# Kernel optimization log

Measured on AMD Instinct MI355X. Metric: run time of the kernel, lower is better.

The kernel has to match this reference:

```python
import jax, jax.numpy as jnp
import numpy as np

# dims
B, S, V, H, D, I, L, SL, P = 1, 2048, 32000, 1024, 512, 4096, 2, 32, 4096
DECAY_FAST, DECAY_SLOW, CONS_RATE, CONS_EVERY = 0.9, 0.99, 0.1, 10


def _ln(x, g, b):
    m = x.mean(-1, keepdims=True)
    v = ((x - m) ** 2).mean(-1, keepdims=True)
    return (x - m) * jax.lax.rsqrt(v + 1e-5) * g + b


def _memory_scan(items, gates, fast0, slow0):
    # items [B,S,D], gates [B,S,SL]; sequential per-timestep memory update
    cons = (jnp.arange(items.shape[1]) % CONS_EVERY) == 0
    def step(carry, x):
        fast, slow = carry
        item, gate, c = x
        fast = DECAY_FAST * fast + gate[:, :, None] * item[:, None, :]
        slow = jnp.where(c, DECAY_SLOW * slow + CONS_RATE * fast, slow)
        fast = jnp.where(c, (1.0 - CONS_RATE) * fast, fast)
        return (fast, slow), None
    (fast, slow), _ = jax.lax.scan(
        step, (fast0, slow0),
        (items.transpose(1, 0, 2), gates.transpose(1, 0, 2), cons))
    return fast, slow


def _forward(input_ids, fast_states, slow_states, emb, pos_emb, W_item, b_item,
             W_q, b_q, rh_W1, rh_b1, rh_W2, rh_b2, gate_W, gate_b, W_out, b_out,
             ln1_g, ln1_b, ffn_W1, ffn_b1, ffn_W2, ffn_b2, ln2_g, ln2_b, fln_g, fln_b):
    b, s = input_ids.shape
    h = emb[input_ids] + pos_emb[:s][None]  # [B,S,H]
    new_fast, new_slow = [], []
    for l in range(W_item.shape[0]):
        items = h @ W_item[l] + b_item[l]          # [B,S,D]
        query = h @ W_q[l] + b_q[l]                # [B,S,H]
        # retrieval head -> unit-norm unbinding keys
        k1 = jax.nn.gelu(items @ rh_W1[l] + rh_b1[l])
        keys = k1 @ rh_W2[l] + rh_b2[l]
        keys = keys / (jnp.linalg.norm(keys, axis=-1, keepdims=True) + 1e-6)
        fast0, slow0 = fast_states[l], slow_states[l]  # [B,SL,D]
        # retrieval uses the initial (constant-within-sequence) states, so it
        # vectorizes over seq: slot attention + hadamard unbinding
        mem = jnp.concatenate([fast0, slow0], axis=1)  # [B,2*SL,D]
        scores = jnp.einsum('bsd,bnd->bsn', keys, mem) / jnp.sqrt(jnp.float32(D))
        attn = jax.nn.softmax(scores, axis=-1)
        retrieved = jnp.einsum('bsn,bnd->bsd', attn, mem) * keys  # [B,S,D]
        gates = jax.nn.sigmoid(jnp.concatenate([h, retrieved], -1) @ gate_W[l] + gate_b[l])
        fast_gates = gates[..., :SL]
        fast, slow = _memory_scan(items, fast_gates, fast0, slow0)
        new_fast.append(fast)
        new_slow.append(slow)
        out = jnp.concatenate([query, retrieved], -1) @ W_out[l] + b_out[l]
        h = _ln(h + out, ln1_g[l], ln1_b[l])
        ffn = jax.nn.gelu(h @ ffn_W1[l] + ffn_b1[l]) @ ffn_W2[l] + ffn_b2[l]
        h = _ln(h + ffn, ln2_g[l], ln2_b[l])
    h = _ln(h, fln_g, fln_b)
    logits = jnp.einsum('bsh,vh->bsv', h, emb)  # tied lm_head
    return logits, jnp.stack(new_fast), jnp.stack(new_slow)


def setup_inputs() -> dict:
    key = jax.random.key(0)
    def rn(i, shape, scale=0.02):
        return jax.random.normal(jax.random.fold_in(key, i), shape, dtype=jnp.float32) * scale
    z = lambda shape: jnp.zeros(shape, jnp.float32)
    return dict(
        input_ids=jax.random.randint(jax.random.fold_in(key, 0), (B, S), 0, V),
        fast_states=rn(100, (L, B, SL, D), 0.5),
        slow_states=rn(101, (L, B, SL, D), 0.5),
        emb=rn(1, (V, H)),
        pos_emb=rn(2, (P, H)),
        W_item=rn(3, (L, H, D)), b_item=z((L, D)),
        W_q=rn(4, (L, H, H)), b_q=z((L, H)),
        rh_W1=rn(5, (L, D, 2 * D)), rh_b1=z((L, 2 * D)),
        rh_W2=rn(6, (L, 2 * D, D)), rh_b2=z((L, D)),
        gate_W=rn(7, (L, H + D, 2 * SL)), gate_b=z((L, 2 * SL)),
        W_out=rn(8, (L, H + D, H)), b_out=z((L, H)),
        ln1_g=jnp.ones((L, H)), ln1_b=z((L, H)),
        ffn_W1=rn(9, (L, H, I)), ffn_b1=z((L, I)),
        ffn_W2=rn(10, (L, I, H)), ffn_b2=z((L, H)),
        ln2_g=jnp.ones((L, H)), ln2_b=z((L, H)),
        fln_g=jnp.ones((H,)), fln_b=z((H,)),
    )


def reference(input_ids, fast_states, slow_states, emb, pos_emb, W_item, b_item,
              W_q, b_q, rh_W1, rh_b1, rh_W2, rh_b2, gate_W, gate_b, W_out, b_out,
              ln1_g, ln1_b, ffn_W1, ffn_b1, ffn_W2, ffn_b2, ln2_g, ln2_b, fln_g, fln_b):
    return _forward(input_ids, fast_states, slow_states, emb, pos_emb, W_item, b_item,
                    W_q, b_q, rh_W1, rh_b1, rh_W2, rh_b2, gate_W, gate_b, W_out, b_out,
                    ln1_g, ln1_b, ffn_W1, ffn_b1, ffn_W2, ffn_b2, ln2_g, ln2_b, fln_g, fln_b)
```

## Files before the change

### kernel.cpp

```cpp
#include <hip/hip_runtime.h>
#include <hip/hip_bf16.h>
#include <stdint.h>

typedef __hip_bfloat16 bf16;
typedef float f32x4 __attribute__((ext_vector_type(4)));
typedef short s16x8 __attribute__((ext_vector_type(8)));
typedef short s16x4 __attribute__((ext_vector_type(4)));

#define DEV __device__ __forceinline__

static constexpr int S_ = 2048, H_ = 1024, D_ = 512, I_ = 4096, V_ = 32000;
static constexpr int SLn = 32, Lc = 2;
static constexpr size_t LOGITS_N = (size_t)S_ * V_;

DEV float gelu_f(float x) {
    float x3 = x * x * x;
    return 0.5f * x * (1.f + tanhf(0.7978845608028654f * (x + 0.044715f * x3)));
}

#define AS1(p) ((const __attribute__((address_space(1))) void*)(uintptr_t)(p))
#define AS3(p) ((__attribute__((address_space(3))) void*)(uint32_t)(uintptr_t)(p))

__global__ __launch_bounds__(512, 1) void logits_gemm(const bf16* __restrict__ A,
                                                      const bf16* __restrict__ BT,
                                                      float* __restrict__ C) {
    constexpr int NT = 32;
    __shared__ short lds[4 * 16384];
    const int tid = threadIdx.x, lane = tid & 63;
    const int wid = tid >> 6;
    const int wm = wid >> 2, wn = wid & 3;

    int bid = blockIdx.x;
    int wgid = (bid & 7) * 125 + (bid >> 3);
    const int m0 = (wgid & 7) * 256;
    const int n0 = (wgid >> 3) * 256;

    const int L = tid * 16;
    const int sidx = L >> 10, w = L & 1023;
    const int r16 = w >> 6;
    const int c2 = (w & 63) ^ (((r16 >> 3) & 1) << 5);
    const int srow = sidx * 16 + r16;
    const int scol = c2 >> 1;
    const bf16* aSrc[2];
    const bf16* bSrc[2];
#pragma unroll
    for (int h = 0; h < 2; ++h) {
        aSrc[h] = A + (size_t)(m0 + h * 128 + srow) * 1536 + scol;
        bSrc[h] = BT + (size_t)(n0 + h * 128 + srow) * 1024 + scol;
    }
    auto STA = [&](int kt, int h) {
        __builtin_amdgcn_global_load_lds(AS1(aSrc[h] + kt * 32),
                                         AS3(&lds[(kt & 3) * 16384 + h * 4096 + tid * 8]), 16, 0, 0);
    };
    auto STB = [&](int kt, int h) {
        __builtin_amdgcn_global_load_lds(AS1(bSrc[h] + kt * 32),
                                         AS3(&lds[(kt & 3) * 16384 + 8192 + h * 4096 + tid * 8]), 16, 0, 0);
    };

    const int laneoff = (lane & 15) * 32 + (((lane >> 4) * 8) ^ (((lane >> 3) & 1) << 4));

    f32x4 acc[8][4];
#pragma unroll
    for (int i = 0; i < 8; i++)
#pragma unroll
        for (int j = 0; j < 4; j++)
#pragma unroll
            for (int r = 0; r < 4; r++) acc[i][j][r] = 0.f;

    s16x8 a0[4], a1[4], b0[4], b1[4];
    auto rdA = [&](s16x8(&d)[4], int kt, int mq) {
        const short* p = &lds[(kt & 3) * 16384 + wm * 4096 + mq * 2048];
#pragma unroll
        for (int f = 0; f < 4; ++f) d[f] = *(const s16x8*)&p[f * 512 + laneoff];
    };
    auto rdB = [&](s16x8(&d)[4], int kt) {
        const short* p = &lds[(kt & 3) * 16384 + 8192 + wn * 2048];
#pragma unroll
        for (int j = 0; j < 4; ++j) d[j] = *(const s16x8*)&p[j * 512 + laneoff];
    };
    auto MM = [&](int mq, s16x8(&a)[4], s16x8(&b)[4]) {
        __builtin_amdgcn_s_setprio(1);
#pragma unroll
        for (int f = 0; f < 4; ++f)
#pragma unroll
            for (int j = 0; j < 4; ++j)
                acc[mq * 4 + f][j] =
                    __builtin_amdgcn_mfma_f32_16x16x32_bf16(a[f], b[j], acc[mq * 4 + f][j], 0, 0, 0);
        __builtin_amdgcn_s_setprio(0);
    };

#define GATE(tight)                                                     \
    do {                                                                \
        __builtin_amdgcn_s_barrier();                                   \
        if (tight) asm volatile("s_waitcnt vmcnt(0)" ::: "memory");     \
        else       asm volatile("s_waitcnt vmcnt(4)" ::: "memory");     \
        asm volatile("s_waitcnt lgkmcnt(0)" ::: "memory");              \
        __builtin_amdgcn_sched_barrier(0);                              \
    } while (0)
#define SB() __builtin_amdgcn_sched_barrier(0)

#pragma unroll
    for (int kt = 0; kt < 3; ++kt) {
        STA(kt, 0); STA(kt, 1); STB(kt, 0); STB(kt, 1);
    }
    asm volatile("s_waitcnt vmcnt(4)" ::: "memory");
    __builtin_amdgcn_s_barrier();
    rdA(a0, 0, 0);
    rdB(b0, 0);

    for (int tt = 0; tt < NT; tt += 2) {
        {
            const int t = tt;
            const bool tight = (t >= NT - 2);
            GATE(tight);
            rdA(a1, t, 1);
            SB();
            MM(0, a0, b0);
            if (t + 3 < NT) { STA(t + 3, 0); STA(t + 3, 1); }
            GATE(tight);
            if (t + 1 < NT) { rdA(a0, t + 1, 0); rdB(b1, t + 1); }
            SB();
            MM(1, a1, b0);
            if (t + 3 < NT) { STB(t + 3, 0); STB(t + 3, 1); }
        }
        {
            const int t = tt + 1;
            const bool tight = (t >= NT - 2);
            GATE(tight);
            rdA(a1, t, 1);
            SB();
            MM(0, a0, b1);
            if (t + 3 < NT) { STA(t + 3, 0); STA(t + 3, 1); }
            GATE(tight);
            if (t + 1 < NT) { rdA(a0, t + 1, 0); rdB(b0, t + 1); }
            SB();
            MM(1, a1, b1);
            if (t + 3 < NT) { STB(t + 3, 0); STB(t + 3, 1); }
        }
    }
#undef GATE
#undef SB

#pragma unroll
    for (int i = 0; i < 8; i++) {
        int gr0 = m0 + wm * 128 + i * 16 + ((lane >> 4) << 2);
#pragma unroll
        for (int j = 0; j < 4; j++) {
            int gc = n0 + wn * 64 + j * 16 + (lane & 15);
#pragma unroll
            for (int r = 0; r < 4; r++) C[(size_t)(gr0 + r) * V_ + gc] = acc[i][j][r];
        }
    }
}

template <int BM, int BN, int TH, int WM, int WN, int FLAGS>
__global__ __launch_bounds__(TH, 3) void gemm_p5(
    const bf16* __restrict__ A, int lda, const bf16* __restrict__ BT,
    const float* __restrict__ bias, const float* __restrict__ bias2,
    float* __restrict__ Cf, int ldf, bf16* __restrict__ Cb, int ldb2,
    bf16* __restrict__ Cb2, int K, int Mt, int Nt) {
    constexpr int FM = BM / (WM * 16), FN = BN / (WN * 16);
    constexpr int CA = (BM * 4) / TH, CB = (BN * 4) / TH, CH = CA + CB;
    constexpr int NPH = (FM * FN >= 32) ? 2 : 1;
    constexpr int FMP = FM / NPH;
    constexpr int BUFS = (BM + BN) * 32;
    __shared__ short lds[4 * BUFS];
    const int tid = threadIdx.x, lane = tid & 63;
    const int wm = (tid >> 6) / WN, wn = (tid >> 6) % WN;

    int nwg = Mt * Nt;
    int bid = blockIdx.x, wgid = bid;
    if ((nwg & 7) == 0) {
        int cpx = nwg >> 3;
        wgid = (bid & 7) * cpx + (bid >> 3);
    }
    const int m0 = (wgid % Mt) * BM, n0 = (wgid / Mt) * BN;

    const bf16* aS[CA];
    const bf16* bS[CB];
#pragma unroll
    for (int c = 0; c < CA; ++c) {
        int L = (c * TH + tid) * 16;
        int sidx = L >> 10, w = L & 1023;
        int r16 = w >> 6;
        int c2 = (w & 63) ^ (((r16 >> 3) & 1) << 5);
        aS[c] = A + (size_t)(m0 + sidx * 16 + r16) * lda + (c2 >> 1);
    }
#pragma unroll
    for (int c = 0; c < CB; ++c) {
        int L = (c * TH + tid) * 16;
        int sidx = L >> 10, w = L & 1023;
        int r16 = w >> 6;
        int c2 = (w & 63) ^ (((r16 >> 3) & 1) << 5);
        bS[c] = BT + (size_t)(n0 + sidx * 16 + r16) * K + (c2 >> 1);
    }

    auto stageA = [&](int kt) {
        short* dst = &lds[(kt & 3) * BUFS];
#pragma unroll
        for (int c = 0; c < CA; ++c)
            __builtin_amdgcn_global_load_lds(AS1(aS[c] + kt * 32), AS3(dst + (c * TH + tid) * 8), 16, 0, 0);
    };
    auto stageB = [&](int kt) {
        short* dst = &lds[(kt & 3) * BUFS + BM * 32];
#pragma unroll
        for (int c = 0; c < CB; ++c)
            __builtin_amdgcn_global_load_lds(AS1(bS[c] + kt * 32), AS3(dst + (c * TH + tid) * 8), 16, 0, 0);
    };

    const int laneoff = ((lane & 15) * 64 + ((((lane >> 4) * 8) ^ (((lane >> 3) & 1) << 4)) << 1)) >> 1;

    f32x4 acc[FM][FN];
#pragma unroll
    for (int i = 0; i < FM; i++)
#pragma unroll
        for (int j = 0; j < FN; j++)
#pragma unroll
            for (int r = 0; r < 4; r++) acc[i][j][r] = 0.f;

    const int NT = K >> 5;
    stageA(0); stageB(0);
    stageA(1); stageB(1);
    stageA(2); stageB(2);
    asm volatile("s_waitcnt vmcnt(%0)" ::"n"(2 * CH) : "memory");
    __builtin_amdgcn_s_barrier();
    for (int t = 0; t < NT; ++t) {
        const short* as = &lds[(t & 3) * BUFS];
        const short* bs = as + BM * 32;
        s16x8 bf[FN];
#pragma unroll
        for (int p = 0; p < NPH; ++p) {
            s16x8 af[FMP];
#pragma unroll
            for (int i = 0; i < FMP; i++)
                af[i] = *(const s16x8*)&as[(wm * FM + p * FMP + i) * 512 + laneoff];
            if (p == 0) {
#pragma unroll
                for (int j = 0; j < FN; j++)
                    bf[j] = *(const s16x8*)&bs[(wn * FN + j) * 512 + laneoff];
            }
            if (t + 3 < NT) {
                if (NPH == 1) {
                    stageA(t + 3);
                    stageB(t + 3);
                } else if (p == 0) {
                    stageA(t + 3);
                } else {
                    stageB(t + 3);
                }
            }
            if (p == NPH - 1) {
                const int rem = NT - 1 - t;
                if (rem >= 3)
                    asm volatile("s_waitcnt vmcnt(%0)" ::"n"(2 * CH) : "memory");
                else if (rem == 2)
                    asm volatile("s_waitcnt vmcnt(%0)" ::"n"(CH) : "memory");
                else
                    asm volatile("s_waitcnt vmcnt(0)" ::: "memory");
            }
            __builtin_amdgcn_s_barrier();
            __builtin_amdgcn_sched_barrier(0);
            __builtin_amdgcn_s_setprio(1);
#pragma unroll
            for (int i = 0; i < FMP; i++)
#pragma unroll
                for (int j = 0; j < FN; j++)
                    acc[p * FMP + i][j] =
                        __builtin_amdgcn_mfma_f32_16x16x32_bf16(af[i], bf[j], acc[p * FMP + i][j], 0, 0, 0);
            __builtin_amdgcn_s_setprio(0);
            __builtin_amdgcn_s_barrier();
        }
    }

#pragma unroll
    for (int i = 0; i < FM; i++) {
        int gr0 = m0 + (wm * FM + i) * 16 + ((lane >> 4) << 2);
#pragma unroll
        for (int j = 0; j < FN; j++) {
            int gc = n0 + (wn * FN + j) * 16 + (lane & 15);
            if (FLAGS & 32) {
                if (gc < 512) {
                    float bv = bias[gc];
#pragma unroll
                    for (int r = 0; r < 4; r++) {
                        float v = acc[i][j][r] + bv;
                        Cf[(size_t)(gr0 + r) * 512 + gc] = v;
                        Cb2[(size_t)(gr0 + r) * 512 + gc] = __float2bfloat16(v);
                    }
                } else {
                    float bv = bias2[gc - 512];
#pragma unroll
                    for (int r = 0; r < 4; r++)
                        Cb[(size_t)(gr0 + r) * 1536 + (gc - 512)] = __float2bfloat16(acc[i][j][r] + bv);
                }
            } else {
                float bv = (FLAGS & 1) ? bias[gc] : 0.f;
#pragma unroll
                for (int r = 0; r < 4; r++) {
                    float v = acc[i][j][r] + bv;
                    if (FLAGS & 2) v = gelu_f(v);
                    if (FLAGS & 4) Cf[(size_t)(gr0 + r) * ldf + gc] = v;
                    if (FLAGS & 8) Cb[(size_t)(gr0 + r) * ldb2 + gc] = __float2bfloat16(v);
                }
            }
        }
    }
}

__global__ __launch_bounds__(256) void transpose_bf16_kernel(const float* __restrict__ W,
                                                             bf16* __restrict__ WT, int K, int N) {
    __shared__ float t[32][33];
    int tx = threadIdx.x & 31, ty = threadIdx.x >> 5;
    int kb = blockIdx.y * 32, nb = blockIdx.x * 32;
#pragma unroll
    for (int i = 0; i < 4; i++)
        t[ty + 8 * i][tx] = W[(size_t)(kb + ty + 8 * i) * N + nb + tx];
    __syncthreads();
#pragma unroll
    for (int i = 0; i < 4; i++)
        WT[(size_t)(nb + ty + 8 * i) * K + kb + tx] = __float2bfloat16(t[tx][ty + 8 * i]);
}

__global__ void conv_bf16_kernel(const float* __restrict__ src, bf16* __restrict__ dst) {
    size_t i = (size_t)blockIdx.x * 256 + threadIdx.x;
    f32x4 v = ((const f32x4*)src)[i];
    s16x4 o;
#pragma unroll
    for (int j = 0; j < 4; j++) {
        bf16 h = __float2bfloat16(v[j]);
        o[j] = *(short*)&h;
    }
    ((s16x4*)dst)[i] = o;
}

__global__ void embed_kernel(const int* __restrict__ ids, const float* __restrict__ emb,
                             const float* __restrict__ pos, float* __restrict__ hF,
                             bf16* __restrict__ hB) {
    int t = blockIdx.x, tid = threadIdx.x;
    int id = ids[t];
    f32x4 v = ((const f32x4*)(emb + (size_t)id * H_))[tid];
    f32x4 q = ((const f32x4*)(pos + (size_t)t * H_))[tid];
    v = v + q;
    ((f32x4*)(hF + (size_t)t * H_))[tid] = v;
    s16x4 o;
#pragma unroll
    for (int j = 0; j < 4; j++) {
        bf16 h = __float2bfloat16(v[j]);
        o[j] = *(short*)&h;
    }
    ((s16x4*)(hB + (size_t)t * 1536))[tid] = o;
}

__global__ __launch_bounds__(256) void ln_kernel(const float* __restrict__ x,
                                                 const float* __restrict__ res,
                                                 const float* __restrict__ g,
                                                 const float* __restrict__ b,
                                                 float* __restrict__ of, bf16* __restrict__ ob,
                                                 int ldo) {
    __shared__ float red[8];
    int row = blockIdx.x, tid = threadIdx.x, lane = tid & 63, wid = tid >> 6;
    const float* xr = x + (size_t)row * H_;
    float v[4];
#pragma unroll
    for (int j = 0; j < 4; j++) {
        int c = tid + 256 * j;
        v[j] = xr[c] + (res ? res[(size_t)row * H_ + c] : 0.f);
    }
    float s = v[0] + v[1] + v[2] + v[3];
#pragma unroll
    for (int o = 32; o; o >>= 1) s += __shfl_xor(s, o);
    if (!lane) red[wid] = s;
    __syncthreads();
    float mean = (red[0] + red[1] + red[2] + red[3]) * (1.f / H_);
    float q = 0.f;
#pragma unroll
    for (int j = 0; j < 4; j++) {
        float d = v[j] - mean;
        q += d * d;
    }
#pragma unroll
    for (int o = 32; o; o >>= 1) q += __shfl_xor(q, o);
    if (!lane) red[4 + wid] = q;
    __syncthreads();
    float var = (red[4] + red[5] + red[6] + red[7]) * (1.f / H_);
    float rstd = rsqrtf(var + 1e-5f);
#pragma unroll
    for (int j = 0; j < 4; j++) {
        int c = tid + 256 * j;
        float o2 = (v[j] - mean) * rstd * g[c] + b[c];
        if (of) of[(size_t)row * H_ + c] = o2;
        if (ob) ob[(size_t)row * ldo + c] = __float2bfloat16(o2);
    }
}

__global__ void memt_kernel(const float* __restrict__ fast0, const float* __restrict__ slow0,
                            float* __restrict__ memT) {
    int idx = blockIdx.x * 256 + threadIdx.x;
    int d = idx >> 6, n = idx & 63;
    const float* m = (n < 32) ? fast0 + (size_t)n * D_ : slow0 + (size_t)(n - 32) * D_;
    memT[idx] = m[d];
}

__global__ __launch_bounds__(256) void attn_kernel(const float* __restrict__ keys,
                                                   const float* __restrict__ memT,
                                                   const float* __restrict__ fast0,
                                                   const float* __restrict__ slow0,
                                                   bf16* __restrict__ qr, bf16* __restrict__ hr) {
    __shared__ float klds[4][512];
    int wid = threadIdx.x >> 6, lane = threadIdx.x & 63;
    int r = blockIdx.x * 4 + wid;
    float kv[8], ss = 0.f;
#pragma unroll
    for (int j = 0; j < 8; j++) {
        kv[j] = keys[(size_t)r * D_ + lane + 64 * j];
        ss += kv[j] * kv[j];
    }
#pragma unroll
    for (int o = 32; o; o >>= 1) ss += __shfl_xor(ss, o);
    float inv = 1.f / (sqrtf(ss) + 1e-6f);
#pragma unroll
    for (int j = 0; j < 8; j++) {
        kv[j] *= inv;
        klds[wid][lane + 64 * j] = kv[j];
    }
    __syncthreads();
    float s0 = 0.f, s1 = 0.f, s2 = 0.f, s3 = 0.f;
#pragma unroll 8
    for (int d = 0; d < 512; d += 4) {
        s0 = fmaf(klds[wid][d + 0], memT[(d + 0) * 64 + lane], s0);
        s1 = fmaf(klds[wid][d + 1], memT[(d + 1) * 64 + lane], s1);
        s2 = fmaf(klds[wid][d + 2], memT[(d + 2) * 64 + lane], s2);
        s3 = fmaf(klds[wid][d + 3], memT[(d + 3) * 64 + lane], s3);
    }
    float s = (s0 + s1 + s2 + s3) * 0.044194173824159216f;
    float m = s;
#pragma unroll
    for (int o = 32; o; o >>= 1) m = fmaxf(m, __shfl_xor(m, o));
    float p = expf(s - m);
    float sum = p;
#pragma unroll
    for (int o = 32; o; o >>= 1) sum += __shfl_xor(sum, o);
    float pn = p / sum;
    float rv[8];
#pragma unroll
    for (int j = 0; j < 8; j++) rv[j] = 0.f;
    for (int n2 = 0; n2 < 64; ++n2) {
        float a2 = __shfl(pn, n2);
        const float* m2 = (n2 < 32) ? (fast0 + (size_t)n2 * D_) : (slow0 + (size_t)(n2 - 32) * D_);
#pragma unroll
        for (int j = 0; j < 8; j++) rv[j] = fmaf(a2, m2[lane + 64 * j], rv[j]);
    }
#pragma unroll
    for (int j = 0; j < 8; j++) {
        bf16 o = __float2bfloat16(rv[j] * kv[j]);
        qr[(size_t)r * 1536 + 1024 + lane + 64 * j] = o;
        hr[(size_t)r * 1536 + 1024 + lane + 64 * j] = o;
    }
}

__global__ void coef_kernel(float* __restrict__ coef) {
    int t = blockIdx.x * 256 + threadIdx.x;
    int j0 = (t + 9) / 10;
    float a = powf(0.9f, (float)(2047 - t + 205 - j0));
    float b = 0.f;
    for (int j = j0; j < 205; ++j)
        b += powf(0.9f, (float)(10 * j - t + j - j0)) * powf(0.99f, (float)(204 - j));
    b *= 0.1f;
    coef[t] = a;
    coef[2048 + t] = b;
    if (t == 0) {
        coef[4096] = powf(0.99f, 205.f);
        float cfs = 0.f;
        for (int j = 0; j < 205; ++j)
            cfs += powf(0.9f, (float)(11 * j + 1)) * powf(0.99f, (float)(204 - j));
        coef[4097] = 0.1f * cfs;
    }
}

__global__ void sigcoef_kernel(const float* __restrict__ raw, const float* __restrict__ coef,
                               float* __restrict__ ga, float* __restrict__ gb) {
    int i = blockIdx.x * 256 + threadIdx.x;
    int r = i >> 5, n = i & 31;
    float g = 1.f / (1.f + expf(-raw[r * 64 + n]));
    ga[i] = g * coef[r];
    gb[i] = g * coef[2048 + r];
}

__global__ __launch_bounds__(256) void scan_part_kernel(const float* __restrict__ items,
                                                        const float* __restrict__ ga,
                                                        const float* __restrict__ gb,
                                                        float* __restrict__ pF,
                                                        float* __restrict__ pS) {
    int tid = threadIdx.x;
    int d = (blockIdx.x & 7) * 64 + (tid & 63);
    int mg = (blockIdx.x >> 3) & 1;
    int tc = blockIdx.x >> 4;
    int m0 = mg * 16 + (tid >> 6) * 4;
    float aF[4] = {0.f, 0.f, 0.f, 0.f}, aS[4] = {0.f, 0.f, 0.f, 0.f};
    for (int t = tc * 128; t < tc * 128 + 128; ++t) {
        float it = items[(size_t)t * D_ + d];
#pragma unroll
        for (int j = 0; j < 4; j++) {
            aF[j] = fmaf(ga[t * 32 + m0 + j], it, aF[j]);
            aS[j] = fmaf(gb[t * 32 + m0 + j], it, aS[j]);
        }
    }
#pragma unroll
    for (int j = 0; j < 4; j++) {
        pF[((size_t)tc * 32 + m0 + j) * D_ + d] = aF[j];
        pS[((size_t)tc * 32 + m0 + j) * D_ + d] = aS[j];
    }
}

__global__ __launch_bounds__(256) void scan_reduce_kernel(const float* __restrict__ pF,
                                                          const float* __restrict__ pS,
                                                          const float* __restrict__ coef,
                                                          const float* __restrict__ fast0,
                                                          const float* __restrict__ slow0,
                                                          float* __restrict__ fastO,
                                                          float* __restrict__ slowO) {
    int i = blockIdx.x * 256 + threadIdx.x;
    float f = 0.f, s = 0.f;
#pragma unroll
    for (int c = 0; c < 16; c++) {
        f += pF[(size_t)c * 32 * D_ + i];
        s += pS[(size_t)c * 32 * D_ + i];
    }
    fastO[i] = f;
    slowO[i] = s + coef[4096] * slow0[i] + coef[4097] * fast0[i];
}

static inline void gemmM(hipStream_t st, const bf16* A, int lda, const bf16* BT,
                         const float* bias, const float* bias2, float* Cf, int ldf, bf16* Cb,
                         int ldb2, bf16* Cb2, int M, int N, int K, int flags) {
    if (N >= 1536 && (N % 128) == 0) {
        int Mt = M / 128, Nt = N / 128;
        dim3 g(Mt * Nt), b(256);
        if (flags == 33)
            gemm_p5<128, 128, 256, 2, 2, 33><<<g, b, 0, st>>>(A, lda, BT, bias, bias2, Cf, ldf,
                                                              Cb, ldb2, Cb2, K, Mt, Nt);
        else if (flags == 11)
            gemm_p5<128, 128, 256, 2, 2, 11><<<g, b, 0, st>>>(A, lda, BT, bias, bias2, Cf, ldf,
                                                              Cb, ldb2, Cb2, K, Mt, Nt);
        else
            gemm_p5<128, 128, 256, 2, 2, 5><<<g, b, 0, st>>>(A, lda, BT, bias, bias2, Cf, ldf,
                                                             Cb, ldb2, Cb2, K, Mt, Nt);
        return;
    }
    int Mt = M / 128, Nt = N / 64;
    dim3 g(Mt * Nt), b(256);
    if (flags == 11)
        gemm_p5<128, 64, 256, 2, 2, 11><<<g, b, 0, st>>>(A, lda, BT, bias, bias2, Cf, ldf, Cb,
                                                         ldb2, Cb2, K, Mt, Nt);
    else
        gemm_p5<128, 64, 256, 2, 2, 5><<<g, b, 0, st>>>(A, lda, BT, bias, bias2, Cf, ldf, Cb,
                                                        ldb2, Cb2, K, Mt, Nt);
}

static inline void transp(hipStream_t st, const float* W, bf16* WT, int K, int N) {
    transpose_bf16_kernel<<<dim3(N / 32, K / 32), 256, 0, st>>>(W, WT, K, N);
}

extern "C" void kernel_launch(void* const* d_in, const int* in_sizes, int n_in,
                              void* d_out, int out_size, void* d_ws, size_t ws_size,
                              hipStream_t stream) {
    const int* ids = (const int*)d_in[0];
    const float* fastS = (const float*)d_in[1];
    const float* slowS = (const float*)d_in[2];
    const float* emb = (const float*)d_in[3];
    const float* pos = (const float*)d_in[4];
    const float* W_item = (const float*)d_in[5];
    const float* b_item = (const float*)d_in[6];
    const float* W_q = (const float*)d_in[7];
    const float* b_q = (const float*)d_in[8];
    const float* rh_W1 = (const float*)d_in[9];
    const float* rh_b1 = (const float*)d_in[10];
    const float* rh_W2 = (const float*)d_in[11];
    const float* rh_b2 = (const float*)d_in[12];
    const float* gate_W = (const float*)d_in[13];
    const float* gate_b = (const float*)d_in[14];
    const float* W_out = (const float*)d_in[15];
    const float* b_out = (const float*)d_in[16];
    const float* ln1_g = (const float*)d_in[17];
    const float* ln1_b = (const float*)d_in[18];
    const float* ffn_W1 = (const float*)d_in[19];
    const float* ffn_b1 = (const float*)d_in[20];
    const float* ffn_W2 = (const float*)d_in[21];
    const float* ffn_b2 = (const float*)d_in[22];
    const float* ln2_g = (const float*)d_in[23];
    const float* ln2_b = (const float*)d_in[24];
    const float* fln_g = (const float*)d_in[25];
    const float* fln_b = (const float*)d_in[26];
    float* outP = (float*)d_out;

    size_t off = 0;
    char* base = (char*)d_ws;
    auto alloc = [&](size_t n) -> char* {
        char* p = base + off;
        off += (n + 255) & ~(size_t)255;
        return p;
    };
    bf16* wIQ = (bf16*)alloc((size_t)Lc * 1536 * H_ * 2);
    bf16* rh1T = (bf16*)alloc((size_t)Lc * (2 * D_) * D_ * 2);
    bf16* rh2T = (bf16*)alloc((size_t)Lc * D_ * (2 * D_) * 2);
    bf16* wOutT = (bf16*)alloc((size_t)Lc * H_ * 1536 * 2);
    bf16* f1T = (bf16*)alloc((size_t)Lc * I_ * H_ * 2);
    bf16* f2T = (bf16*)alloc((size_t)Lc * H_ * I_ * 2);
    bf16* gWT = (bf16*)alloc((size_t)Lc * 64 * 1536 * 2);
    bf16* embB = (bf16*)alloc((size_t)V_ * H_ * 2);
    float* hF = (float*)alloc((size_t)S_ * H_ * 4);
    bf16* hrB = (bf16*)alloc((size_t)S_ * 1536 * 2);
    bf16* hB = hrB;
    float* itemsF = (float*)alloc((size_t)S_ * D_ * 4);
    bf16* itemsB = (bf16*)alloc((size_t)S_ * D_ * 2);
    bf16* qrB = (bf16*)alloc((size_t)S_ * 1536 * 2);
    bf16* k1B = (bf16*)alloc((size_t)S_ * (2 * D_) * 2);
    float* keysF = (float*)alloc((size_t)S_ * D_ * 4);
    float* outF = (float*)alloc((size_t)S_ * H_ * 4);
    bf16* ffn1B = (bf16*)alloc((size_t)S_ * I_ * 2);
    float* gRawF = (float*)alloc((size_t)S_ * 64 * 4);
    float* gaF = (float*)alloc((size_t)S_ * SLn * 4);
    float* gbF = (float*)alloc((size_t)S_ * SLn * 4);
    float* coefF = (float*)alloc(4200 * 4);
    float* memT = (float*)alloc((size_t)D_ * 64 * 4);
    float* pF = (float*)alloc((size_t)16 * SLn * D_ * 4);
    float* pS = (float*)alloc((size_t)16 * SLn * D_ * 4);

    coef_kernel<<<8, 256, 0, stream>>>(coefF);
    for (int l = 0; l < Lc; ++l) {
        transp(stream, W_item + (size_t)l * H_ * D_, wIQ + (size_t)l * 1536 * H_, H_, D_);
        transp(stream, W_q + (size_t)l * H_ * H_, wIQ + (size_t)l * 1536 * H_ + (size_t)512 * H_,
               H_, H_);
        transp(stream, rh_W1 + (size_t)l * D_ * 2 * D_, rh1T + (size_t)l * 2 * D_ * D_, D_, 2 * D_);
        transp(stream, rh_W2 + (size_t)l * 2 * D_ * D_, rh2T + (size_t)l * D_ * 2 * D_, 2 * D_, D_);
        transp(stream, W_out + (size_t)l * 1536 * H_, wOutT + (size_t)l * H_ * 1536, 1536, H_);
        transp(stream, ffn_W1 + (size_t)l * H_ * I_, f1T + (size_t)l * I_ * H_, H_, I_);
        transp(stream, ffn_W2 + (size_t)l * I_ * H_, f2T + (size_t)l * H_ * I_, I_, H_);
        transp(stream, gate_W + (size_t)l * 1536 * 64, gWT + (size_t)l * 64 * 1536, 1536, 64);
    }
    conv_bf16_kernel<<<(int)((size_t)V_ * H_ / 4 / 256), 256, 0, stream>>>(emb, embB);
    embed_kernel<<<S_, 256, 0, stream>>>(ids, emb, pos, hF, hB);

    for (int l = 0; l < Lc; ++l) {
        const float* fast0 = fastS + (size_t)l * SLn * D_;
        const float* slow0 = slowS + (size_t)l * SLn * D_;
        gemmM(stream, hB, 1536, wIQ + (size_t)l * 1536 * H_, b_item + l * D_, b_q + l * H_,
              itemsF, 512, qrB, 1536, itemsB, S_, 1536, H_, 33);
        gemmM(stream, itemsB, D_, rh1T + (size_t)l * 2 * D_ * D_, rh_b1 + l * 2 * D_, nullptr,
              nullptr, 0, k1B, 2 * D_, nullptr, S_, 2 * D_, D_, 11);
        gemmM(stream, k1B, 2 * D_, rh2T + (size_t)l * D_ * 2 * D_, rh_b2 + l * D_, nullptr,
              keysF, D_, nullptr, 0, nullptr, S_, D_, 2 * D_, 5);
        memt_kernel<<<128, 256, 0, stream>>>(fast0, slow0, memT);
        attn_kernel<<<S_ / 4, 256, 0, stream>>>(keysF, memT, fast0, slow0, qrB, hrB);
        gemmM(stream, hrB, 1536, gWT + (size_t)l * 64 * 1536, gate_b + l * 64, nullptr, gRawF,
              64, nullptr, 0, nullptr, S_, 64, 1536, 5);
        sigcoef_kernel<<<S_ * SLn / 256, 256, 0, stream>>>(gRawF, coefF, gaF, gbF);
        scan_part_kernel<<<256, 256, 0, stream>>>(itemsF, gaF, gbF, pF, pS);
        scan_reduce_kernel<<<64, 256, 0, stream>>>(
            pF, pS, coefF, fast0, slow0, outP + LOGITS_N + (size_t)l * SLn * D_,
            outP + LOGITS_N + (size_t)Lc * SLn * D_ + (size_t)l * SLn * D_);
        gemmM(stream, qrB, 1536, wOutT + (size_t)l * H_ * 1536, b_out + l * H_, nullptr, outF,
              H_, nullptr, 0, nullptr, S_, H_, 1536, 5);
        ln_kernel<<<S_, 256, 0, stream>>>(hF, outF, ln1_g + l * H_, ln1_b + l * H_, hF, hB, 1536);
        gemmM(stream, hB, 1536, f1T + (size_t)l * I_ * H_, ffn_b1 + l * I_, nullptr, nullptr, 0,
              ffn1B, I_, nullptr, S_, I_, H_, 11);
        gemmM(stream, ffn1B, I_, f2T + (size_t)l * H_ * I_, ffn_b2 + l * H_, nullptr, outF, H_,
              nullptr, 0, nullptr, S_, H_, I_, 5);
        ln_kernel<<<S_, 256, 0, stream>>>(hF, outF, ln2_g + l * H_, ln2_b + l * H_, hF, hB, 1536);
    }
    ln_kernel<<<S_, 256, 0, stream>>>(hF, nullptr, fln_g, fln_b, nullptr, hB, 1536);
    logits_gemm<<<1000, 512, 0, stream>>>(hB, embB, outP);
}
```

Measured before the change: 887.6 us.

## Restructure logits GEMM main loop to one barrier per k-tile with full-tile register double-buffering

The logits GEMM main loop now reads whole k-tiles (8 A fragments and 4 B fragments) into alternating even/odd register sets. Each k-tile gets one barrier/waitcnt gate instead of two half-tile gates. The A and B global-to-LDS loads for a stage are issued together. The vmcnt wait now comes before the barrier rather than after it. The aim is to cut synchronisation overhead and give longer uninterrupted MFMA runs, at the cost of more operand registers live at once and a coarser overlap between LDS reads and MFMAs.

```diff
diff --git a/kernel.cpp b/kernel.cpp
--- a/kernel.cpp
+++ b/kernel.cpp
@@ -48,13 +48,14 @@
         aSrc[h] = A + (size_t)(m0 + h * 128 + srow) * 1536 + scol;
         bSrc[h] = BT + (size_t)(n0 + h * 128 + srow) * 1024 + scol;
     }
-    auto STA = [&](int kt, int h) {
-        __builtin_amdgcn_global_load_lds(AS1(aSrc[h] + kt * 32),
-                                         AS3(&lds[(kt & 3) * 16384 + h * 4096 + tid * 8]), 16, 0, 0);
-    };
-    auto STB = [&](int kt, int h) {
-        __builtin_amdgcn_global_load_lds(AS1(bSrc[h] + kt * 32),
-                                         AS3(&lds[(kt & 3) * 16384 + 8192 + h * 4096 + tid * 8]), 16, 0, 0);
+    auto stage = [&](int kt) {
+#pragma unroll
+        for (int h = 0; h < 2; ++h) {
+            __builtin_amdgcn_global_load_lds(AS1(aSrc[h] + kt * 32),
+                                             AS3(&lds[(kt & 3) * 16384 + h * 4096 + tid * 8]), 16, 0, 0);
+            __builtin_amdgcn_global_load_lds(AS1(bSrc[h] + kt * 32),
+                                             AS3(&lds[(kt & 3) * 16384 + 8192 + h * 4096 + tid * 8]), 16, 0, 0);
+        }
     };
 
     const int laneoff = (lane & 15) * 32 + (((lane >> 4) * 8) ^ (((lane >> 3) & 1) << 4));
@@ -67,76 +68,70 @@
 #pragma unroll
             for (int r = 0; r < 4; r++) acc[i][j][r] = 0.f;
 
-    s16x8 a0[4], a1[4], b0[4], b1[4];
-    auto rdA = [&](s16x8(&d)[4], int kt, int mq) {
-        const short* p = &lds[(kt & 3) * 16384 + wm * 4096 + mq * 2048];
-#pragma unroll
-        for (int f = 0; f < 4; ++f) d[f] = *(const s16x8*)&p[f * 512 + laneoff];
-    };
-    auto rdB = [&](s16x8(&d)[4], int kt) {
-        const short* p = &lds[(kt & 3) * 16384 + 8192 + wn * 2048];
-#pragma unroll
-        for (int j = 0; j < 4; ++j) d[j] = *(const s16x8*)&p[j * 512 + laneoff];
-    };
-    auto MM = [&](int mq, s16x8(&a)[4], s16x8(&b)[4]) {
+    s16x8 aE[8], bE[4], aO[8], bO[4];
+    auto readE = [&](int kt) {
+        const short* pa = &lds[(kt & 3) * 16384 + wm * 4096];
+#pragma unroll
+        for (int f = 0; f < 8; ++f) aE[f] = *(const s16x8*)&pa[(f >> 2) * 2048 + (f & 3) * 512 + laneoff];
+        const short* pb = &lds[(kt & 3) * 16384 + 8192 + wn * 2048];
+#pragma unroll
+        for (int j = 0; j < 4; ++j) bE[j] = *(const s16x8*)&pb[j * 512 + laneoff];
+    };
+    auto readO = [&](int kt) {
+        const short* pa = &lds[(kt & 3) * 16384 + wm * 4096];
+#pragma unroll
+        for (int f = 0; f < 8; ++f) aO[f] = *(const s16x8*)&pa[(f >> 2) * 2048 + (f & 3) * 512 + laneoff];
+        const short* pb = &lds[(kt & 3) * 16384 + 8192 + wn * 2048];
+#pragma unroll
+        for (int j = 0; j < 4; ++j) bO[j] = *(const s16x8*)&pb[j * 512 + laneoff];
+    };
+    auto MM2E = [&]() {
         __builtin_amdgcn_s_setprio(1);
 #pragma unroll
-        for (int f = 0; f < 4; ++f)
+        for (int f = 0; f < 8; ++f)
 #pragma unroll
             for (int j = 0; j < 4; ++j)
-                acc[mq * 4 + f][j] =
-                    __builtin_amdgcn_mfma_f32_16x16x32_bf16(a[f], b[j], acc[mq * 4 + f][j], 0, 0, 0);
+                acc[f][j] = __builtin_amdgcn_mfma_f32_16x16x32_bf16(aE[f], bE[j], acc[f][j], 0, 0, 0);
+        __builtin_amdgcn_s_setprio(0);
+    };
+    auto MM2O = [&]() {
+        __builtin_amdgcn_s_setprio(1);
+#pragma unroll
+        for (int f = 0; f < 8; ++f)
+#pragma unroll
+            for (int j = 0; j < 4; ++j)
+                acc[f][j] = __builtin_amdgcn_mfma_f32_16x16x32_bf16(aO[f], bO[j], acc[f][j], 0, 0, 0);
         __builtin_amdgcn_s_setprio(0);
     };
 
 #define GATE(tight)                                                     \
     do {                                                                \
-        __builtin_amdgcn_s_barrier();                                   \
         if (tight) asm volatile("s_waitcnt vmcnt(0)" ::: "memory");     \
         else       asm volatile("s_waitcnt vmcnt(4)" ::: "memory");     \
+        __builtin_amdgcn_s_barrier();                                   \
         asm volatile("s_waitcnt lgkmcnt(0)" ::: "memory");              \
         __builtin_amdgcn_sched_barrier(0);                              \
     } while (0)
 #define SB() __builtin_amdgcn_sched_barrier(0)
 
-#pragma unroll
-    for (int kt = 0; kt < 3; ++kt) {
-        STA(kt, 0); STA(kt, 1); STB(kt, 0); STB(kt, 1);
-    }
-    asm volatile("s_waitcnt vmcnt(4)" ::: "memory");
+    stage(0);
+    stage(1);
+    stage(2);
+    asm volatile("s_waitcnt vmcnt(8)" ::: "memory");
     __builtin_amdgcn_s_barrier();
-    rdA(a0, 0, 0);
-    rdB(b0, 0);
-
-    for (int tt = 0; tt < NT; tt += 2) {
-        {
-            const int t = tt;
-            const bool tight = (t >= NT - 2);
-            GATE(tight);
-            rdA(a1, t, 1);
-            SB();
-            MM(0, a0, b0);
-            if (t + 3 < NT) { STA(t + 3, 0); STA(t + 3, 1); }
-            GATE(tight);
-            if (t + 1 < NT) { rdA(a0, t + 1, 0); rdB(b1, t + 1); }
-            SB();
-            MM(1, a1, b0);
-            if (t + 3 < NT) { STB(t + 3, 0); STB(t + 3, 1); }
-        }
-        {
-            const int t = tt + 1;
-            const bool tight = (t >= NT - 2);
-            GATE(tight);
-            rdA(a1, t, 1);
-            SB();
-            MM(0, a0, b1);
-            if (t + 3 < NT) { STA(t + 3, 0); STA(t + 3, 1); }
-            GATE(tight);
-            if (t + 1 < NT) { rdA(a0, t + 1, 0); rdB(b0, t + 1); }
-            SB();
-            MM(1, a1, b1);
-            if (t + 3 < NT) { STB(t + 3, 0); STB(t + 3, 1); }
-        }
+    readE(0);
+
+    for (int t = 0; t < NT; t += 2) {
+        GATE(t >= NT - 2);
+        readO(t + 1);
+        SB();
+        MM2E();
+        if (t + 3 < NT) stage(t + 3);
+        GATE(t + 1 >= NT - 2);
+        if (t + 2 < NT) readE(t + 2);
+        SB();
+        MM2O();
+        if (t + 4 < NT) stage(t + 4);
     }
 #undef GATE
 #undef SB
```

New measurement: 901.7 us. About the same (+1.6%).
